# Optimization experiments

Hardware: AMD Instinct MI355X
Metric: run time of the kernel (lower is better)

## Reference

```python
import jax, jax.numpy as jnp
import numpy as np

B, T, D, H = 2, 2048, 1024, 16
HD = D // H  # 64
EPS = 1e-5

def _ln(x, g, b):
    mu = jnp.mean(x, axis=-1, keepdims=True)
    var = jnp.mean(jnp.square(x - mu), axis=-1, keepdims=True)
    return (x - mu) * jax.lax.rsqrt(var + EPS) * g + b

def setup_inputs() -> dict:
    key = jax.random.key(0)
    ks = jax.random.split(key, 12)
    s = 0.02
    return {
        "x":  jax.random.normal(ks[0], (B, T, D), jnp.float32),
        "Wq": jax.random.normal(ks[1], (H, D, HD), jnp.float32) * s,
        "Wk": jax.random.normal(ks[2], (H, D, HD), jnp.float32) * s,
        "Wv": jax.random.normal(ks[3], (H, D, HD), jnp.float32) * s,
        "Wo": jax.random.normal(ks[4], (D, D), jnp.float32) * s,
        "bo": jnp.zeros((D,), jnp.float32),
        "W1": jax.random.normal(ks[5], (D, 4 * D), jnp.float32) * s,
        "b1": jnp.zeros((4 * D,), jnp.float32),
        "W2": jax.random.normal(ks[6], (4 * D, D), jnp.float32) * s,
        "b2": jnp.zeros((D,), jnp.float32),
        "ln1_g": jnp.ones((D,), jnp.float32),
        "ln1_b": jnp.zeros((D,), jnp.float32),
        "ln2_g": jnp.ones((D,), jnp.float32),
        "ln2_b": jnp.zeros((D,), jnp.float32),
    }

def reference(x, Wq, Wk, Wv, Wo, bo, W1, b1, W2, b2, ln1_g, ln1_b, ln2_g, ln2_b):
    b, t, d = x.shape
    # --- self-attention on ln1(x) ---
    h = _ln(x, ln1_g, ln1_b)
    q = jnp.einsum('btd,hde->bhte', h, Wq)  # [B,H,T,hd]
    k = jnp.einsum('btd,hde->bhte', h, Wk)
    v = jnp.einsum('btd,hde->bhte', h, Wv)
    # NOTE: original code scales by C**-0.5 with C = N_EMBED (not head_size)
    wei = jnp.einsum('bhte,bhse->bhts', q, k) * (d ** -0.5)
    causal = jnp.tril(jnp.ones((t, t), bool))
    wei = jnp.where(causal, wei, -jnp.inf)
    att = jax.nn.softmax(wei, axis=-1)
    o = jnp.einsum('bhts,bhse->bhte', att, v)
    o = o.transpose(0, 2, 1, 3).reshape(b, t, d)  # concat heads
    x = x + o @ Wo + bo
    # --- feed-forward on ln2(x) ---
    h2 = _ln(x, ln2_g, ln2_b)
    ff = jax.nn.relu(h2 @ W1 + b1) @ W2 + b2
    return x + ff
```

## Files before the change

kernel.cpp:

```cpp
#include <hip/hip_runtime.h>
#include <stdint.h>

typedef unsigned short u16;
typedef __attribute__((ext_vector_type(8))) short bf16x8;
typedef __attribute__((ext_vector_type(4))) float f32x4;
typedef __attribute__((ext_vector_type(4))) unsigned int u32x4;
typedef __attribute__((ext_vector_type(2))) unsigned int u32x2;
typedef __attribute__((ext_vector_type(4))) unsigned short u16x4;

#define MFMA16(a, b, c) __builtin_amdgcn_mfma_f32_16x16x32_bf16(a, b, c, 0, 0, 0)
#define VMCNT(N) asm volatile("s_waitcnt vmcnt(" #N ")" ::: "memory")

__device__ __forceinline__ u16 f2bf(float f) {
  union { float f; uint32_t u; } v; v.f = f;
  uint32_t r = v.u + 0x7FFFu + ((v.u >> 16) & 1u);
  return (u16)(r >> 16);
}

__device__ __forceinline__ float bf2f(u16 u) {
  union { uint32_t u; float f; } v; v.u = ((uint32_t)u) << 16;
  return v.f;
}

__device__ __forceinline__ uint32_t cvt_pk_bf16(float a, float b) {
  uint32_t r;
  asm("v_cvt_pk_bf16_f32 %0, %1, %2" : "=v"(r) : "v"(a), "v"(b));
  return r;
}

__device__ __forceinline__ void gload_lds16(const u16* g, u16* l) {
  __builtin_amdgcn_global_load_lds((const __attribute__((address_space(1))) void*)(g),
                                   (__attribute__((address_space(3))) void*)(l), 16, 0, 0);
}

__global__ __launch_bounds__(256) void ln_kernel(const float* __restrict__ x,
                                                 const float* __restrict__ g,
                                                 const float* __restrict__ beta,
                                                 u16* __restrict__ out) {
  int row = blockIdx.x;
  int tid = threadIdx.x;
  float4 v = ((const float4*)(x + (size_t)row * 1024))[tid];
  float s = v.x + v.y + v.z + v.w;
  float ss = v.x * v.x + v.y * v.y + v.z * v.z + v.w * v.w;
#pragma unroll
  for (int m = 1; m < 64; m <<= 1) { s += __shfl_xor(s, m); ss += __shfl_xor(ss, m); }
  __shared__ float red[8];
  int wave = tid >> 6, lane = tid & 63;
  if (lane == 0) { red[wave] = s; red[4 + wave] = ss; }
  __syncthreads();
  s = red[0] + red[1] + red[2] + red[3];
  ss = red[4] + red[5] + red[6] + red[7];
  float mean = s * (1.0f / 1024.0f);
  float var = ss * (1.0f / 1024.0f) - mean * mean;
  float rstd = rsqrtf(var + 1e-5f);
  float4 gv = ((const float4*)g)[tid];
  float4 bv = ((const float4*)beta)[tid];
  u16x4 o;
  o.x = f2bf((v.x - mean) * rstd * gv.x + bv.x);
  o.y = f2bf((v.y - mean) * rstd * gv.y + bv.y);
  o.z = f2bf((v.z - mean) * rstd * gv.z + bv.z);
  o.w = f2bf((v.w - mean) * rstd * gv.w + bv.w);
  *(u16x4*)(out + (size_t)row * 1024 + tid * 4) = o;
}

__global__ __launch_bounds__(256) void transpose_f32_bf16(const float* __restrict__ in,
                                                          u16* __restrict__ out,
                                                          int K, int N,
                                                          size_t in_bstride, size_t out_bstride) {
  __shared__ float tile[32][33];
  const float* I = in + (size_t)blockIdx.z * in_bstride;
  u16* O = out + (size_t)blockIdx.z * out_bstride;
  int n0 = blockIdx.x * 32, k0 = blockIdx.y * 32;
  int tx = threadIdx.x & 31, ty = threadIdx.x >> 5;
#pragma unroll
  for (int i = 0; i < 4; i++)
    tile[ty + i * 8][tx] = I[(size_t)(k0 + ty + i * 8) * N + n0 + tx];
  __syncthreads();
#pragma unroll
  for (int i = 0; i < 4; i++)
    O[(size_t)(n0 + ty + i * 8) * K + k0 + tx] = f2bf(tile[tx][ty + i * 8]);
}

template <int EP>
__global__ __launch_bounds__(512, 2) void gemm8p(const u16* __restrict__ A,
                                                 const u16* __restrict__ Bt,
                                                 int M, int N, int K, int KS,
                                                 void* __restrict__ out0,
                                                 u16* __restrict__ out1,
                                                 u16* __restrict__ out2,
                                                 const float* __restrict__ bias) {
  __shared__ __align__(16) u16 lds[65536];
  const int tid = threadIdx.x;
  const int lane = tid & 63, wave = tid >> 6;
  const int lo = lane & 15, hi = lane >> 4;
  const int wm = wave >> 2, wn = wave & 3;
  int gx = gridDim.x;
  int lin = blockIdx.y * gx + blockIdx.x;
  int nwg = gx * gridDim.y;
  int cpx = nwg >> 3;
  int swz = (lin & 7) * cpx + (lin >> 3);
  int bm0 = (swz / gx) * 256, bn0 = (swz % gx) * 256;
  int kbeg = blockIdx.z * KS;
  int T = KS >> 6;

  int rs_ = tid >> 3, ss_ = (tid & 7) ^ (rs_ & 7);
  const u16* srcA = A + (size_t)(bm0 + rs_) * K + kbeg + ss_ * 8;
  const u16* srcB = Bt + (size_t)(bn0 + rs_) * K + kbeg + ss_ * 8;
  const size_t i1 = (size_t)64 * K;
  const size_t h1 = (size_t)128 * K;
  const int dst0 = wave * 512;
  const int dst1 = 4096 + wave * 512;

  const int rpA = wm * 16 + lo;
  const int rpB = wn * 16 + lo;
  const int sp0 = (hi ^ (lo & 7)) * 8;

  f32x4 acc[8][4] = {};
  bf16x8 a[4][2], b0[2][2], b1[2][2];

  auto stageA = [&](int buf, int h, int koff) {
    const u16* s = srcA + koff + (h ? h1 : 0);
    u16* d = lds + (buf * 2 + h) * 8192;
    gload_lds16(s, d + dst0);
    gload_lds16(s + i1, d + dst1);
  };
  auto stageB = [&](int buf, int h, int koff) {
    const u16* s = srcB + koff + (h ? h1 : 0);
    u16* d = lds + 32768 + (buf * 2 + h) * 8192;
    gload_lds16(s, d + dst0);
    gload_lds16(s + i1, d + dst1);
  };
  auto loadA = [&](int buf, int h) {
    const u16* base = lds + (buf * 2 + h) * 8192 + rpA * 64;
#pragma unroll
    for (int m = 0; m < 4; m++) {
      a[m][0] = *(const bf16x8*)(base + m * 2048 + sp0);
      a[m][1] = *(const bf16x8*)(base + m * 2048 + (sp0 ^ 32));
    }
  };
  auto loadB = [&](bf16x8 (&bb)[2][2], int buf, int g) {
    const u16* base = lds + 32768 + (buf * 2 + g) * 8192 + rpB * 64;
#pragma unroll
    for (int n = 0; n < 2; n++) {
      bb[n][0] = *(const bf16x8*)(base + n * 4096 + sp0);
      bb[n][1] = *(const bf16x8*)(base + n * 4096 + (sp0 ^ 32));
    }
  };
  auto mmac = [&](int mh, int np, bf16x8 (&bb)[2][2]) {
    __builtin_amdgcn_s_setprio(1);
#pragma unroll
    for (int m = 0; m < 4; m++)
#pragma unroll
      for (int n = 0; n < 2; n++) {
        acc[mh + m][np + n] = MFMA16(a[m][0], bb[n][0], acc[mh + m][np + n]);
        acc[mh + m][np + n] = MFMA16(a[m][1], bb[n][1], acc[mh + m][np + n]);
      }
    __builtin_amdgcn_s_setprio(0);
  };

  stageA(0, 0, 0); stageB(0, 0, 0); stageB(0, 1, 0); stageA(0, 1, 0);
  VMCNT(4);
  __builtin_amdgcn_s_barrier();

  int koff = 64;
  for (int t = 0; t < T - 1; ++t) {
    int cur = t & 1, nxt = cur ^ 1;
    loadA(cur, 0); loadB(b0, cur, 0);
    stageA(nxt, 0, koff);
    VMCNT(4);
    __builtin_amdgcn_s_barrier();
    mmac(0, 0, b0);
    loadB(b1, cur, 1);
    stageB(nxt, 0, koff);
    VMCNT(4);
    __builtin_amdgcn_s_barrier();
    mmac(0, 2, b1);
    loadA(cur, 1);
    stageB(nxt, 1, koff);
    __builtin_amdgcn_s_barrier();
    mmac(4, 0, b0);
    stageA(nxt, 1, koff);
    VMCNT(4);
    __builtin_amdgcn_s_barrier();
    mmac(4, 2, b1);
    koff += 64;
  }
  {
    int cur = (T - 1) & 1;
    loadA(cur, 0); loadB(b0, cur, 0);
    VMCNT(2);
    __builtin_amdgcn_s_barrier();
    mmac(0, 0, b0);
    loadB(b1, cur, 1);
    VMCNT(0);
    __builtin_amdgcn_s_barrier();
    mmac(0, 2, b1);
    loadA(cur, 1);
    __builtin_amdgcn_s_barrier();
    mmac(4, 0, b0);
    mmac(4, 2, b1);
  }

#pragma unroll
  for (int mt = 0; mt < 8; mt++) {
    int gr0 = bm0 + (mt >> 2) * 128 + (mt & 3) * 32 + wm * 16 + hi * 4;
#pragma unroll
    for (int nt = 0; nt < 4; nt++) {
      int gc = bn0 + (nt >> 1) * 128 + (nt & 1) * 64 + wn * 16 + lo;
#pragma unroll
      for (int j = 0; j < 4; j++) {
        int gr = gr0 + j;
        float val = acc[mt][nt][j];
        if constexpr (EP == 0) {
          int b_ = gr >> 11, t_ = gr & 2047;
          int sec = gc >> 10, nn = gc & 1023, h_ = nn >> 6, e_ = nn & 63;
          size_t bh = (size_t)(b_ * 16 + h_);
          if (sec == 0)      ((u16*)out0)[(bh * 2048 + t_) * 64 + e_] = f2bf(val * 0.0450842200f);
          else if (sec == 1) out1[(bh * 2048 + t_) * 64 + e_] = f2bf(val);
          else               out2[(bh * 64 + e_) * 2048 + t_] = f2bf(val);
        } else if constexpr (EP == 2) {
          float v = val + bias[gc];
          ((u16*)out0)[(size_t)gr * N + gc] = f2bf(fmaxf(v, 0.0f));
        } else if constexpr (EP == 4) {
          ((u16*)out0)[(size_t)blockIdx.z * M * N + (size_t)gr * N + gc] = f2bf(val);
        }
      }
    }
  }
}

__global__ __launch_bounds__(256) void combine4(float* __restrict__ out,
                                                const float* __restrict__ res,
                                                const u16* __restrict__ p,
                                                const float* __restrict__ bias) {
  size_t i = ((size_t)blockIdx.x * 256 + threadIdx.x) * 4;
  float4 r = *(const float4*)(res + i);
  float4 bb = *(const float4*)(bias + (i & 1023));
  float a0 = r.x + bb.x, a1 = r.y + bb.y, a2 = r.z + bb.z, a3 = r.w + bb.w;
#pragma unroll
  for (int z = 0; z < 4; z++) {
    u16x4 v = *(const u16x4*)(p + (size_t)z * 4096 * 1024 + i);
    a0 += bf2f(v.x); a1 += bf2f(v.y); a2 += bf2f(v.z); a3 += bf2f(v.w);
  }
  float4 o4 = {a0, a1, a2, a3};
  *(float4*)(out + i) = o4;
}

__global__ __launch_bounds__(512, 4) void attn_kernel(const u16* __restrict__ q,
                                                      const u16* __restrict__ k,
                                                      const u16* __restrict__ vt,
                                                      u16* __restrict__ o) {
  __shared__ __align__(16) u16 Ks[2][64 * 64];
  __shared__ __align__(16) u16 Vs[2][64 * 64];
  __shared__ __align__(16) u16 Ps[8][16 * 72];
  int bh = blockIdx.y;
  int pi = blockIdx.x;
  int tid = threadIdx.x, lane = tid & 63, wave = tid >> 6;
  int lo = lane & 15, hi = lane >> 4;
  int grp = wave >> 2;
  int qblk_w = grp ? pi : (31 - pi);
  int qb0 = qblk_w * 64;
  int nkb = 32 - pi;
  const u16* qbase = q + (size_t)bh * 2048 * 64;
  const u16* kbase = k + (size_t)bh * 2048 * 64;
  const u16* vbase = vt + (size_t)bh * 64 * 2048;

  int srow = tid >> 3;
  int ssl = (tid & 7) ^ (srow & 7);
  int kOff = srow * 64 + ssl * 8;
  int vOff = srow * 2048 + ssl * 8;

  int qrow = qb0 + (wave & 3) * 16 + lo;
  bf16x8 qf0 = *(const bf16x8*)(qbase + (size_t)qrow * 64 + hi * 8);
  bf16x8 qf1 = *(const bf16x8*)(qbase + (size_t)qrow * 64 + 32 + hi * 8);

  float l_r = 0.0f;
  f32x4 of[4] = {};
  u16* Pw = Ps[wave];

  auto stage = [&](int b, int kb) {
    gload_lds16(kbase + (size_t)kb * 4096 + kOff, Ks[b] + wave * 512);
    gload_lds16(vbase + kb * 64 + vOff, Vs[b] + wave * 512);
  };

  stage(0, 0);
  __syncthreads();

  for (int kb = 0; kb < nkb; kb++) {
    int cur = kb & 1;
    if (kb + 1 < nkb) stage(cur ^ 1, kb + 1);
    if (kb <= qblk_w) {
      const u16* Kb = Ks[cur];
      const u16* Vb = Vs[cur];
      f32x4 s4[4] = {};
#pragma unroll
      for (int nt = 0; nt < 4; nt++) {
        int r = nt * 16 + lo, rw = r & 7;
        bf16x8 kf0 = *(const bf16x8*)(Kb + r * 64 + ((hi ^ rw) << 3));
        bf16x8 kf1 = *(const bf16x8*)(Kb + r * 64 + (((hi + 4) ^ rw) << 3));
        s4[nt] = MFMA16(kf0, qf0, s4[nt]);
        s4[nt] = MFMA16(kf1, qf1, s4[nt]);
      }
      float rs = 0.0f;
      bool diag = (kb == qblk_w);
#pragma unroll
      for (int nt = 0; nt < 4; nt++) {
        float e0, e1, e2, e3;
        if (diag) {
          int key = kb * 64 + nt * 16 + hi * 4;
          e0 = (key     > qrow) ? 0.0f : __builtin_amdgcn_exp2f(s4[nt][0]);
          e1 = (key + 1 > qrow) ? 0.0f : __builtin_amdgcn_exp2f(s4[nt][1]);
          e2 = (key + 2 > qrow) ? 0.0f : __builtin_amdgcn_exp2f(s4[nt][2]);
          e3 = (key + 3 > qrow) ? 0.0f : __builtin_amdgcn_exp2f(s4[nt][3]);
        } else {
          e0 = __builtin_amdgcn_exp2f(s4[nt][0]);
          e1 = __builtin_amdgcn_exp2f(s4[nt][1]);
          e2 = __builtin_amdgcn_exp2f(s4[nt][2]);
          e3 = __builtin_amdgcn_exp2f(s4[nt][3]);
        }
        rs += (e0 + e1) + (e2 + e3);
        u32x2 w;
        w.x = cvt_pk_bf16(e0, e1);
        w.y = cvt_pk_bf16(e2, e3);
        *(u32x2*)(Pw + lo * 72 + nt * 16 + hi * 4) = w;
      }
      rs += __shfl_xor(rs, 16);
      rs += __shfl_xor(rs, 32);
      l_r += rs;
      bf16x8 pb0 = *(const bf16x8*)(Pw + lo * 72 + hi * 8);
      bf16x8 pb1 = *(const bf16x8*)(Pw + lo * 72 + 32 + hi * 8);
#pragma unroll
      for (int et = 0; et < 4; et++) {
        int e = et * 16 + lo, ew = e & 7;
        bf16x8 v0 = *(const bf16x8*)(Vb + e * 64 + ((hi ^ ew) << 3));
        bf16x8 v1 = *(const bf16x8*)(Vb + e * 64 + (((hi + 4) ^ ew) << 3));
        of[et] = MFMA16(v0, pb0, of[et]);
        of[et] = MFMA16(v1, pb1, of[et]);
      }
    }
    __syncthreads();
  }
  int hh = bh & 15, bb = bh >> 4;
  float inv = 1.0f / l_r;
  size_t obase = ((size_t)(bb * 2048 + qrow)) * 1024 + hh * 64 + hi * 4;
#pragma unroll
  for (int et = 0; et < 4; et++) {
    u32x2 w;
    w.x = cvt_pk_bf16(of[et][0] * inv, of[et][1] * inv);
    w.y = cvt_pk_bf16(of[et][2] * inv, of[et][3] * inv);
    *(u32x2*)(o + obase + et * 16) = w;
  }
}

extern "C" void kernel_launch(void* const* d_in, const int* in_sizes, int n_in,
                              void* d_out, int out_size, void* d_ws, size_t ws_size,
                              hipStream_t stream) {
  const float* x = (const float*)d_in[0];
  const float* Wq = (const float*)d_in[1];
  const float* Wk = (const float*)d_in[2];
  const float* Wv = (const float*)d_in[3];
  const float* Wo = (const float*)d_in[4];
  const float* bo = (const float*)d_in[5];
  const float* W1 = (const float*)d_in[6];
  const float* b1 = (const float*)d_in[7];
  const float* W2 = (const float*)d_in[8];
  const float* b2 = (const float*)d_in[9];
  const float* g1 = (const float*)d_in[10];
  const float* be1 = (const float*)d_in[11];
  const float* g2 = (const float*)d_in[12];
  const float* be2 = (const float*)d_in[13];
  float* out = (float*)d_out;
  char* ws = (char*)d_ws;
  const size_t MB = 1024ull * 1024ull;

  u16* h = (u16*)(ws + 0);
  u16* o = h;
  u16* BtQKV = (u16*)(ws + 8 * MB);
  u16* WoT = BtQKV;
  u16* qb = (u16*)(ws + 14 * MB);
  u16* kb = (u16*)(ws + 22 * MB);
  u16* vtb = (u16*)(ws + 30 * MB);
  u16* h2 = vtb;
  u16* pwo = (u16*)(ws + 14 * MB);
  u16* W1T = (u16*)(ws + 38 * MB);
  u16* W2T = W1T;
  u16* yb = (u16*)(ws + 46 * MB);
  u16* pf2 = (u16*)(ws + 0);

  ln_kernel<<<4096, 256, 0, stream>>>(x, g1, be1, h);
  transpose_f32_bf16<<<dim3(2, 32, 16), 256, 0, stream>>>(Wq, BtQKV, 1024, 64,
                                                          (size_t)1024 * 64, (size_t)64 * 1024);
  transpose_f32_bf16<<<dim3(2, 32, 16), 256, 0, stream>>>(Wk, BtQKV + 1024 * 1024, 1024, 64,
                                                          (size_t)1024 * 64, (size_t)64 * 1024);
  transpose_f32_bf16<<<dim3(2, 32, 16), 256, 0, stream>>>(Wv, BtQKV + 2048 * 1024, 1024, 64,
                                                          (size_t)1024 * 64, (size_t)64 * 1024);
  gemm8p<0><<<dim3(12, 16), 512, 0, stream>>>(h, BtQKV, 4096, 3072, 1024, 1024,
                                              (void*)qb, kb, vtb, nullptr);
  attn_kernel<<<dim3(16, 32), 512, 0, stream>>>(qb, kb, vtb, o);
  transpose_f32_bf16<<<dim3(32, 32, 1), 256, 0, stream>>>(Wo, WoT, 1024, 1024, 0, 0);
  gemm8p<4><<<dim3(4, 16, 4), 512, 0, stream>>>(o, WoT, 4096, 1024, 1024, 256,
                                                (void*)pwo, nullptr, nullptr, nullptr);
  combine4<<<4096, 256, 0, stream>>>(out, x, pwo, bo);
  ln_kernel<<<4096, 256, 0, stream>>>(out, g2, be2, h2);
  transpose_f32_bf16<<<dim3(128, 32, 1), 256, 0, stream>>>(W1, W1T, 1024, 4096, 0, 0);
  gemm8p<2><<<dim3(16, 16), 512, 0, stream>>>(h2, W1T, 4096, 4096, 1024, 1024,
                                              (void*)yb, nullptr, nullptr, b1);
  transpose_f32_bf16<<<dim3(32, 128, 1), 256, 0, stream>>>(W2, W2T, 4096, 1024, 0, 0);
  gemm8p<4><<<dim3(4, 16, 4), 512, 0, stream>>>(yb, W2T, 4096, 1024, 4096, 1024,
                                                (void*)pf2, nullptr, nullptr, nullptr);
  combine4<<<4096, 256, 0, stream>>>(out, out, pf2, b2);
}
```

Before: 235.7 us.

## Fuse residual combine with LayerNorm, restructure GEMM pipeline sync, vectorize V-transpose stores

Replaces the separate combine4 and second ln_kernel launches with one combine_ln kernel that adds the residual, bias and split-K partials, then computes LayerNorm in registers. This avoids one launch and one full read of the fp32 activations. The GEMM main loop is folded into a single loop with a guarded last iteration, and gains extra barriers, explicit lgkmcnt waits and sched_barriers around each MFMA group, which may add synchronization overhead. The QKV epilogue hoists the section test per block and writes the transposed V output as packed 4-element bf16 stores.

```diff
diff --git a/kernel.cpp b/kernel.cpp
--- a/kernel.cpp
+++ b/kernel.cpp
@@ -10,6 +10,7 @@
 
 #define MFMA16(a, b, c) __builtin_amdgcn_mfma_f32_16x16x32_bf16(a, b, c, 0, 0, 0)
 #define VMCNT(N) asm volatile("s_waitcnt vmcnt(" #N ")" ::: "memory")
+#define LGKM0() asm volatile("s_waitcnt lgkmcnt(0)" ::: "memory")
 
 __device__ __forceinline__ u16 f2bf(float f) {
   union { float f; uint32_t u; } v; v.f = f;
@@ -61,6 +62,48 @@
   o.z = f2bf((v.z - mean) * rstd * gv.z + bv.z);
   o.w = f2bf((v.w - mean) * rstd * gv.w + bv.w);
   *(u16x4*)(out + (size_t)row * 1024 + tid * 4) = o;
+}
+
+__global__ __launch_bounds__(256) void combine_ln(const float* __restrict__ x,
+                                                  const u16* __restrict__ p,
+                                                  const float* __restrict__ bo,
+                                                  const float* __restrict__ g,
+                                                  const float* __restrict__ beta,
+                                                  float* __restrict__ out,
+                                                  u16* __restrict__ h2) {
+  int row = blockIdx.x;
+  int tid = threadIdx.x;
+  size_t i = (size_t)row * 1024 + tid * 4;
+  float4 v = *(const float4*)(x + i);
+  float4 bb = *(const float4*)(bo + tid * 4);
+  v.x += bb.x; v.y += bb.y; v.z += bb.z; v.w += bb.w;
+#pragma unroll
+  for (int z = 0; z < 4; z++) {
+    u16x4 pv = *(const u16x4*)(p + (size_t)z * 4096 * 1024 + i);
+    v.x += bf2f(pv.x); v.y += bf2f(pv.y); v.z += bf2f(pv.z); v.w += bf2f(pv.w);
+  }
+  *(float4*)(out + i) = v;
+  float s = v.x + v.y + v.z + v.w;
+  float ss = v.x * v.x + v.y * v.y + v.z * v.z + v.w * v.w;
+#pragma unroll
+  for (int m = 1; m < 64; m <<= 1) { s += __shfl_xor(s, m); ss += __shfl_xor(ss, m); }
+  __shared__ float red[8];
+  int wave = tid >> 6, lane = tid & 63;
+  if (lane == 0) { red[wave] = s; red[4 + wave] = ss; }
+  __syncthreads();
+  s = red[0] + red[1] + red[2] + red[3];
+  ss = red[4] + red[5] + red[6] + red[7];
+  float mean = s * (1.0f / 1024.0f);
+  float var = ss * (1.0f / 1024.0f) - mean * mean;
+  float rstd = rsqrtf(var + 1e-5f);
+  float4 gv = ((const float4*)g)[tid];
+  float4 bv = ((const float4*)beta)[tid];
+  u16x4 o;
+  o.x = f2bf((v.x - mean) * rstd * gv.x + bv.x);
+  o.y = f2bf((v.y - mean) * rstd * gv.y + bv.y);
+  o.z = f2bf((v.z - mean) * rstd * gv.z + bv.z);
+  o.w = f2bf((v.w - mean) * rstd * gv.w + bv.w);
+  *(u16x4*)(h2 + i) = o;
 }
 
 __global__ __launch_bounds__(256) void transpose_f32_bf16(const float* __restrict__ in,
@@ -162,67 +205,71 @@
   VMCNT(4);
   __builtin_amdgcn_s_barrier();
 
-  int koff = 64;
-  for (int t = 0; t < T - 1; ++t) {
+  for (int t = 0; t < T; ++t) {
     int cur = t & 1, nxt = cur ^ 1;
+    bool more = (t + 1 < T);
+    int koff = (t + 1) * 64;
     loadA(cur, 0); loadB(b0, cur, 0);
-    stageA(nxt, 0, koff);
-    VMCNT(4);
-    __builtin_amdgcn_s_barrier();
+    if (more) stageA(nxt, 0, koff);
+    __builtin_amdgcn_s_barrier();
+    LGKM0();
+    __builtin_amdgcn_sched_barrier(0);
     mmac(0, 0, b0);
+    __builtin_amdgcn_s_barrier();
     loadB(b1, cur, 1);
-    stageB(nxt, 0, koff);
-    VMCNT(4);
-    __builtin_amdgcn_s_barrier();
+    if (more) { stageB(nxt, 0, koff); VMCNT(6); } else { VMCNT(2); }
+    __builtin_amdgcn_s_barrier();
+    LGKM0();
+    __builtin_amdgcn_sched_barrier(0);
     mmac(0, 2, b1);
+    __builtin_amdgcn_s_barrier();
     loadA(cur, 1);
-    stageB(nxt, 1, koff);
-    __builtin_amdgcn_s_barrier();
+    if (more) { stageB(nxt, 1, koff); VMCNT(6); } else { VMCNT(0); }
+    __builtin_amdgcn_s_barrier();
+    LGKM0();
+    __builtin_amdgcn_sched_barrier(0);
     mmac(4, 0, b0);
-    stageA(nxt, 1, koff);
-    VMCNT(4);
+    __builtin_amdgcn_s_barrier();
+    if (more) { stageA(nxt, 1, koff); VMCNT(4); }
     __builtin_amdgcn_s_barrier();
     mmac(4, 2, b1);
-    koff += 64;
-  }
-  {
-    int cur = (T - 1) & 1;
-    loadA(cur, 0); loadB(b0, cur, 0);
-    VMCNT(2);
-    __builtin_amdgcn_s_barrier();
-    mmac(0, 0, b0);
-    loadB(b1, cur, 1);
-    VMCNT(0);
-    __builtin_amdgcn_s_barrier();
-    mmac(0, 2, b1);
-    loadA(cur, 1);
-    __builtin_amdgcn_s_barrier();
-    mmac(4, 0, b0);
-    mmac(4, 2, b1);
-  }
-
+    __builtin_amdgcn_s_barrier();
+  }
+
+  const int sec = (EP == 0) ? (bn0 >> 10) : 0;
 #pragma unroll
   for (int mt = 0; mt < 8; mt++) {
     int gr0 = bm0 + (mt >> 2) * 128 + (mt & 3) * 32 + wm * 16 + hi * 4;
 #pragma unroll
     for (int nt = 0; nt < 4; nt++) {
       int gc = bn0 + (nt >> 1) * 128 + (nt & 1) * 64 + wn * 16 + lo;
-#pragma unroll
-      for (int j = 0; j < 4; j++) {
-        int gr = gr0 + j;
-        float val = acc[mt][nt][j];
-        if constexpr (EP == 0) {
-          int b_ = gr >> 11, t_ = gr & 2047;
-          int sec = gc >> 10, nn = gc & 1023, h_ = nn >> 6, e_ = nn & 63;
-          size_t bh = (size_t)(b_ * 16 + h_);
-          if (sec == 0)      ((u16*)out0)[(bh * 2048 + t_) * 64 + e_] = f2bf(val * 0.0450842200f);
-          else if (sec == 1) out1[(bh * 2048 + t_) * 64 + e_] = f2bf(val);
-          else               out2[(bh * 64 + e_) * 2048 + t_] = f2bf(val);
-        } else if constexpr (EP == 2) {
-          float v = val + bias[gc];
-          ((u16*)out0)[(size_t)gr * N + gc] = f2bf(fmaxf(v, 0.0f));
-        } else if constexpr (EP == 4) {
-          ((u16*)out0)[(size_t)blockIdx.z * M * N + (size_t)gr * N + gc] = f2bf(val);
+      if constexpr (EP == 0) {
+        int b_ = gr0 >> 11, t_ = gr0 & 2047;
+        int nn = gc & 1023, h_ = nn >> 6, e_ = nn & 63;
+        size_t bh = (size_t)(b_ * 16 + h_);
+        if (sec == 2) {
+          u32x2 w;
+          w.x = cvt_pk_bf16(acc[mt][nt][0], acc[mt][nt][1]);
+          w.y = cvt_pk_bf16(acc[mt][nt][2], acc[mt][nt][3]);
+          *(u32x2*)(out2 + (bh * 64 + e_) * 2048 + t_) = w;
+        } else {
+          float sc = (sec == 0) ? 0.0450842200f : 1.0f;
+          u16* dst = (sec == 0) ? (u16*)out0 : out1;
+#pragma unroll
+          for (int j = 0; j < 4; j++)
+            dst[(bh * 2048 + t_ + j) * 64 + e_] = f2bf(acc[mt][nt][j] * sc);
+        }
+      } else {
+#pragma unroll
+        for (int j = 0; j < 4; j++) {
+          int gr = gr0 + j;
+          float val = acc[mt][nt][j];
+          if constexpr (EP == 2) {
+            float v = val + bias[gc];
+            ((u16*)out0)[(size_t)gr * N + gc] = f2bf(fmaxf(v, 0.0f));
+          } else if constexpr (EP == 4) {
+            ((u16*)out0)[(size_t)blockIdx.z * M * N + (size_t)gr * N + gc] = f2bf(val);
+          }
         }
       }
     }
@@ -400,8 +447,7 @@
   transpose_f32_bf16<<<dim3(32, 32, 1), 256, 0, stream>>>(Wo, WoT, 1024, 1024, 0, 0);
   gemm8p<4><<<dim3(4, 16, 4), 512, 0, stream>>>(o, WoT, 4096, 1024, 1024, 256,
                                                 (void*)pwo, nullptr, nullptr, nullptr);
-  combine4<<<4096, 256, 0, stream>>>(out, x, pwo, bo);
-  ln_kernel<<<4096, 256, 0, stream>>>(out, g2, be2, h2);
+  combine_ln<<<4096, 256, 0, stream>>>(x, pwo, bo, g2, be2, out, h2);
   transpose_f32_bf16<<<dim3(128, 32, 1), 256, 0, stream>>>(W1, W1T, 1024, 4096, 0, 0);
   gemm8p<2><<<dim3(16, 16), 512, 0, stream>>>(h2, W1T, 4096, 4096, 1024, 1024,
                                               (void*)yb, nullptr, nullptr, b1);
```

New measurement: 223.1 us. 5.3% less time.
